# Kernel tuning notes

Hardware: AMD Instinct MI355X
Metric: run time of the kernel (lower is better)

## Reference

```python
import jax, jax.numpy as jnp
import numpy as np

B, N, K, H, G, C, P = 2, 8192, 16, 128, 256, 10, 8


def _w(key, fan_in, fan_out):
    return jax.random.normal(key, (fan_in, fan_out), jnp.float32) * (1.0 / np.sqrt(fan_in))


def setup_inputs() -> dict:
    key = jax.random.key(0)
    ks = jax.random.split(key, 24)
    inp = {
        "points": jax.random.normal(ks[0], (B, N, 3), jnp.float32),
        "normals": jax.random.normal(ks[1], (B, N, 3), jnp.float32),
        # point_encoder: Linear(6,H) -> ReLU -> Linear(H,H) -> ReLU
        "We1": _w(ks[2], 6, H), "be1": jnp.zeros((H,), jnp.float32),
        "We2": _w(ks[3], H, H), "be2": jnp.zeros((H,), jnp.float32),
        # local_mlp: Linear(2H,H) -> ReLU -> Linear(H,H) -> ReLU
        "Wl1": _w(ks[4], 2 * H, H), "bl1": jnp.zeros((H,), jnp.float32),
        "Wl2": _w(ks[5], H, H), "bl2": jnp.zeros((H,), jnp.float32),
        # context_proj: Linear(2H,G) -> ReLU
        "Wc": _w(ks[6], 2 * H, G), "bc": jnp.zeros((G,), jnp.float32),
        # classifier: Linear(2H+G,H) -> ReLU -> Linear(H,C)
        "Wk1": _w(ks[7], 2 * H + G, H), "bk1": jnp.zeros((H,), jnp.float32),
        "Wk2": _w(ks[8], H, C), "bk2": jnp.zeros((C,), jnp.float32),
        # param_head: Linear(2H+G,H) -> ReLU -> Linear(H,P)
        "Wp1": _w(ks[9], 2 * H + G, H), "bp1": jnp.zeros((H,), jnp.float32),
        "Wp2": _w(ks[10], H, P), "bp2": jnp.zeros((P,), jnp.float32),
        "k": K,
    }
    return inp


def _knn_indices(points, k):
    # squared pairwise distances (same ordering as torch.cdist); no grad needed
    pts = jax.lax.stop_gradient(points)
    sq = jnp.sum(pts * pts, axis=-1)                      # [B,N]
    d2 = sq[:, :, None] + sq[:, None, :] - 2.0 * jnp.einsum('bnc,bmc->bnm', pts, pts)
    _, idx = jax.lax.top_k(-d2, k + 1)                    # smallest k+1 distances
    return idx[:, :, 1:]                                  # drop self -> [B,N,k]


def _forward(points, normals, We1, be1, We2, be2, Wl1, bl1, Wl2, bl2,
             Wc, bc, Wk1, bk1, Wk2, bk2, Wp1, bp1, Wp2, bp2, k):
    x = jnp.concatenate([points, normals], axis=-1)       # [B,N,6]
    pf = jax.nn.relu(jax.nn.relu(x @ We1 + be1) @ We2 + be2)   # [B,N,H]

    idx = _knn_indices(points, k)                         # [B,N,k]
    nbr = jax.vmap(lambda f, i: f[i])(pf, idx)            # [B,N,k,H]
    ctr = pf[:, :, None, :]
    edge = jnp.concatenate([jnp.broadcast_to(ctr, nbr.shape), nbr - ctr], axis=-1)  # [B,N,k,2H]
    lf = jax.nn.relu(jax.nn.relu(edge @ Wl1 + bl1) @ Wl2 + bl2)
    lf = jnp.max(lf, axis=2)                              # [B,N,H]

    ctx = jax.nn.relu(jnp.concatenate([pf, lf], axis=-1) @ Wc + bc)  # [B,N,G]
    gf = jnp.max(ctx, axis=1, keepdims=True)              # [B,1,G]
    gf = jnp.broadcast_to(gf, (pf.shape[0], pf.shape[1], gf.shape[-1]))

    fused = jnp.concatenate([pf, lf, gf], axis=-1)        # [B,N,2H+G]
    logits = jax.nn.relu(fused @ Wk1 + bk1) @ Wk2 + bk2
    param_pred = jax.nn.relu(fused @ Wp1 + bp1) @ Wp2 + bp2
    return logits, param_pred


def reference(points, normals, We1, be1, We2, be2, Wl1, bl1, Wl2, bl2,
              Wc, bc, Wk1, bk1, Wk2, bk2, Wp1, bp1, Wp2, bp2, k):
    return _forward(points, normals, We1, be1, We2, be2, Wl1, bl1, Wl2, bl2,
                    Wc, bc, Wk1, bk1, Wk2, bk2, Wp1, bp1, Wp2, bp2, k)
```

## Files before the change

### kernel.cpp

```cpp
#include <hip/hip_runtime.h>

#define B_ 2
#define N_ 8192
#define NP 16384
#define K_ 16
#define H_ 128
#define KCAP 512

typedef short bf16x8 __attribute__((ext_vector_type(8)));
typedef float f32x4 __attribute__((ext_vector_type(4)));

__device__ inline unsigned short f2b(float f) {
    unsigned u = __builtin_bit_cast(unsigned, f);
    unsigned r = (u + 0x7fff + ((u >> 16) & 1)) >> 16;
    return (unsigned short)r;
}
__device__ inline bf16x8 ldb8(const unsigned short* p) {
    return *(const bf16x8*)p;
}
__device__ inline uint4 pack8(float4 a, float4 b) {
    uint4 pk;
    pk.x = (unsigned)f2b(a.x) | ((unsigned)f2b(a.y) << 16);
    pk.y = (unsigned)f2b(a.z) | ((unsigned)f2b(a.w) << 16);
    pk.z = (unsigned)f2b(b.x) | ((unsigned)f2b(b.y) << 16);
    pk.w = (unsigned)f2b(b.z) | ((unsigned)f2b(b.w) << 16);
    return pk;
}

__global__ __launch_bounds__(256) void k_h1(
    const float* __restrict__ pts, const float* __restrict__ nrm,
    const float* __restrict__ We1, const float* __restrict__ be1,
    unsigned short* __restrict__ h1, float* __restrict__ gf,
    float4* __restrict__ pts4) {
    int tid = blockIdx.x * 256 + threadIdx.x;
    if (blockIdx.x == 0) { gf[threadIdx.x] = 0.f; gf[256 + threadIdx.x] = 0.f; }
    if (tid < NP) {
        int p = tid;
        float x = pts[p * 3], y = pts[p * 3 + 1], z = pts[p * 3 + 2];
        float sq = __fadd_rn(__fadd_rn(__fmul_rn(x, x), __fmul_rn(y, y)), __fmul_rn(z, z));
        pts4[p] = make_float4(x, y, z, sq);
    }
    for (int o = tid; o < NP * 128; o += gridDim.x * 256) {
        int p = o >> 7, h = o & 127;
        float a = be1[h];
        a += pts[p * 3]     * We1[0 * 128 + h];
        a += pts[p * 3 + 1] * We1[1 * 128 + h];
        a += pts[p * 3 + 2] * We1[2 * 128 + h];
        a += nrm[p * 3]     * We1[3 * 128 + h];
        a += nrm[p * 3 + 1] * We1[4 * 128 + h];
        a += nrm[p * 3 + 2] * We1[5 * 128 + h];
        h1[o] = f2b(fmaxf(a, 0.f));
    }
}

__global__ __launch_bounds__(256) void k_prep(
    const float* __restrict__ Wl1, const float* __restrict__ bl1,
    const float* __restrict__ Wl2, const float* __restrict__ Wc,
    const float* __restrict__ Wk1, const float* __restrict__ Wp1,
    const float* __restrict__ We2,
    unsigned short* __restrict__ WuvT, float* __restrict__ bias_cat,
    unsigned short* __restrict__ Wl2T, unsigned short* __restrict__ WcT,
    unsigned short* __restrict__ Wk1T, unsigned short* __restrict__ Wp1T,
    unsigned short* __restrict__ We2T) {
    int tid = blockIdx.x * 256 + threadIdx.x;
    int stride = gridDim.x * 256;
    for (int i = tid; i < 256 * 128; i += stride) {
        int n = i >> 7, k = i & 127;
        float val = (n < 128) ? Wl1[k * 128 + n] - Wl1[(k + 128) * 128 + n]
                              : Wl1[(k + 128) * 128 + (n - 128)];
        WuvT[i] = f2b(val);
    }
    for (int i = tid; i < 256; i += stride) bias_cat[i] = (i < 128) ? bl1[i] : 0.f;
    for (int i = tid; i < 128 * 128; i += stride) {
        int n = i >> 7, k = i & 127;
        Wl2T[i] = f2b(Wl2[k * 128 + n]);
        We2T[i] = f2b(We2[k * 128 + n]);
    }
    for (int i = tid; i < 256 * 256; i += stride) {
        int n = i >> 8, k = i & 255;
        WcT[i] = f2b(Wc[k * 256 + n]);
    }
    for (int i = tid; i < 128 * 512; i += stride) {
        int n = i >> 9, k = i & 511;
        Wk1T[i] = f2b(Wk1[k * 128 + n]);
        Wp1T[i] = f2b(Wp1[k * 128 + n]);
    }
}

__global__ __launch_bounds__(256) void k_pf2(
    const unsigned short* __restrict__ h1, const unsigned short* __restrict__ We2T,
    const float* __restrict__ be2, float* __restrict__ pf) {
    int t = threadIdx.x, l = t & 63, w = t >> 6;
    int row0 = blockIdx.x * 64 + w * 16;
    f32x4 acc[8];
    #pragma unroll
    for (int nj = 0; nj < 8; ++nj) acc[nj] = (f32x4){0.f, 0.f, 0.f, 0.f};
    #pragma unroll
    for (int ks = 0; ks < 4; ++ks) {
        bf16x8 a = ldb8(&h1[(size_t)(row0 + (l & 15)) * 128 + ks * 32 + (l >> 4) * 8]);
        #pragma unroll
        for (int nj = 0; nj < 8; ++nj) {
            bf16x8 bfr = ldb8(&We2T[(size_t)(nj * 16 + (l & 15)) * 128 + ks * 32 + (l >> 4) * 8]);
            acc[nj] = __builtin_amdgcn_mfma_f32_16x16x32_bf16(a, bfr, acc[nj], 0, 0, 0);
        }
    }
    #pragma unroll
    for (int nj = 0; nj < 8; ++nj) {
        int col = nj * 16 + (l & 15);
        float bias = be2[col];
        #pragma unroll
        for (int rg = 0; rg < 4; ++rg) {
            int row = row0 + (l >> 4) * 4 + rg;
            pf[(size_t)row * 128 + col] = fmaxf(acc[nj][rg] + bias, 0.f);
        }
    }
}

__device__ inline float knn_thresh(const int* __restrict__ hh, int l) {
    int h0 = hh[4 * l], h1 = hh[4 * l + 1], h2 = hh[4 * l + 2], h3 = hh[4 * l + 3];
    int c0 = h0, c1 = c0 + h1, c2 = c1 + h2, c3 = c2 + h3;
    int tot = c3;
    int inc = tot;
    for (int off = 1; off < 64; off <<= 1) {
        int vv = __shfl_up(inc, off);
        if (l >= off) inc += vv;
    }
    int excl = inc - tot;
    int Bc = 255;
    if      (excl + c0 >= 16) Bc = 4 * l;
    else if (excl + c1 >= 16) Bc = 4 * l + 1;
    else if (excl + c2 >= 16) Bc = 4 * l + 2;
    else if (excl + c3 >= 16) Bc = 4 * l + 3;
    for (int m = 1; m < 64; m <<= 1) Bc = min(Bc, __shfl_xor(Bc, m));
    return __uint_as_float((unsigned)(Bc + 401) << 21);
}

__global__ __launch_bounds__(256) void k_knn(
    const float4* __restrict__ pts4, int* __restrict__ knn) {
    __shared__ int hist[4][260];
    __shared__ unsigned long long buf[4][KCAP];
    int t = threadIdx.x, w = t >> 6, l = t & 63;
    int b = blockIdx.x >> 11;
    int q = (blockIdx.x & 2047) * 4 + w;
    const float4* pb = pts4 + b * N_;
    float4 qp = pb[q];
    for (int i = l; i < 256; i += 64) hist[w][i] = 0;
    int cntw = 0;

    #pragma unroll 2
    for (int i = 0; i < 16; ++i) {
        int j = l + 64 * i;
        float4 c = pb[j];
        float dot = __fadd_rn(__fadd_rn(__fmul_rn(qp.x, c.x), __fmul_rn(qp.y, c.y)), __fmul_rn(qp.z, c.z));
        float d2 = __fsub_rn(__fadd_rn(qp.w, c.w), __fmul_rn(2.f, dot));
        d2 = (j == q) ? 1e30f : d2;
        unsigned uu = __float_as_uint(d2);
        int bk = (d2 < 0.f) ? 0 : min(255, max(0, (int)(uu >> 21) - 400));
        atomicAdd(&hist[w][bk], 1);
    }
    float Tf = knn_thresh(&hist[w][0], l);

    #pragma unroll 4
    for (int i = 0; i < 128; ++i) {
        int j = l + 64 * i;
        float4 c = pb[j];
        float dot = __fadd_rn(__fadd_rn(__fmul_rn(qp.x, c.x), __fmul_rn(qp.y, c.y)), __fmul_rn(qp.z, c.z));
        float d2 = __fsub_rn(__fadd_rn(qp.w, c.w), __fmul_rn(2.f, dot));
        bool take = (d2 < Tf);
        unsigned long long mask = __ballot(take);
        if (take) {
            unsigned du = __float_as_uint(d2);
            unsigned mu = du ^ (unsigned)(((int)du >> 31) | 0x80000000);
            int pos = cntw + __popcll(mask & ((1ull << l) - 1ull));
            if (pos < KCAP) buf[w][pos] = ((unsigned long long)mu << 32) | (unsigned)j;
        }
        cntw += __popcll(mask);
    }
    int m_ = min(cntw, KCAP);

    unsigned long long key[8];
    #pragma unroll
    for (int r = 0; r < 8; ++r) {
        int e = l + 64 * r;
        key[r] = (e < m_) ? buf[w][e] : ~0ull;
    }
    unsigned long long lmin = key[0];
    #pragma unroll
    for (int r = 1; r < 8; ++r) lmin = (key[r] < lmin) ? key[r] : lmin;
    int emitted = 0;
    for (int r17 = 0; r17 < 17 && emitted < 16; ++r17) {
        unsigned long long wv = lmin;
        for (int m = 1; m < 64; m <<= 1) {
            unsigned long long o = __shfl_xor(wv, m);
            wv = (o < wv) ? o : wv;
        }
        int idx = (int)(wv & 0xffffffffu);
        if (idx != q) {
            if (l == 0) knn[((size_t)b * N_ + q) * 16 + emitted] = b * N_ + idx;
            ++emitted;
        }
        if (lmin == wv) {
            #pragma unroll
            for (int r = 0; r < 8; ++r) if (key[r] == wv) key[r] = ~0ull;
            lmin = key[0];
            #pragma unroll
            for (int r = 1; r < 8; ++r) lmin = (key[r] < lmin) ? key[r] : lmin;
        }
    }
}

__global__ __launch_bounds__(256) void k_uv(
    const float* __restrict__ pf, const unsigned short* __restrict__ WuvT,
    const float* __restrict__ bias_cat,
    float* __restrict__ u, float* __restrict__ v) {
    __shared__ __align__(16) unsigned short As[128 * 136];
    int t = threadIdx.x;
    int l = t & 63, w = t >> 6;
    int wr = w >> 1, wcn = w & 1;
    int rowbase = blockIdx.x * 128;
    int ncol0 = blockIdx.y * 128;

    #pragma unroll
    for (int i = 0; i < 8; ++i) {
        int ci = t + 256 * i;
        int r = ci >> 4, c8 = (ci & 15) * 8;
        const float4* sp = (const float4*)(pf + (size_t)(rowbase + r) * 128 + c8);
        *(uint4*)&As[r * 136 + c8] = pack8(sp[0], sp[1]);
    }
    __syncthreads();

    f32x4 acc[4][4];
    #pragma unroll
    for (int i = 0; i < 4; ++i)
        #pragma unroll
        for (int j = 0; j < 4; ++j) acc[i][j] = (f32x4){0.f, 0.f, 0.f, 0.f};

    #pragma unroll
    for (int ks = 0; ks < 4; ++ks) {
        bf16x8 bfr[4], afr[4];
        #pragma unroll
        for (int nj = 0; nj < 4; ++nj)
            bfr[nj] = ldb8(&WuvT[(size_t)(ncol0 + wcn * 64 + nj * 16 + (l & 15)) * 128 + ks * 32 + (l >> 4) * 8]);
        #pragma unroll
        for (int mi = 0; mi < 4; ++mi)
            afr[mi] = ldb8(&As[(wr * 64 + mi * 16 + (l & 15)) * 136 + ks * 32 + (l >> 4) * 8]);
        #pragma unroll
        for (int mi = 0; mi < 4; ++mi)
            #pragma unroll
            for (int nj = 0; nj < 4; ++nj)
                acc[mi][nj] = __builtin_amdgcn_mfma_f32_16x16x32_bf16(afr[mi], bfr[nj], acc[mi][nj], 0, 0, 0);
    }
    float* outp = (ncol0 == 0) ? u : v;
    #pragma unroll
    for (int mi = 0; mi < 4; ++mi)
        #pragma unroll
        for (int nj = 0; nj < 4; ++nj) {
            int col = wcn * 64 + nj * 16 + (l & 15);
            float bias = bias_cat[ncol0 + col];
            #pragma unroll
            for (int rg = 0; rg < 4; ++rg) {
                int row = wr * 64 + mi * 16 + (l >> 4) * 4 + rg;
                outp[(size_t)(rowbase + row) * 128 + col] = acc[mi][nj][rg] + bias;
            }
        }
}

__global__ __launch_bounds__(256) void k_edge(
    const float* __restrict__ u, const float* __restrict__ v,
    const int* __restrict__ knn, const unsigned short* __restrict__ Wl2T,
    const float* __restrict__ bl2, float* __restrict__ lf) {
    __shared__ __align__(16) unsigned short h1s[128 * 136];
    int t = threadIdx.x;
    int l = t & 63, w = t >> 6;
    int wr = w >> 1, wcn = w & 1;
    int rowbase = blockIdx.x * 128;
    int p0 = blockIdx.x * 8;

    #pragma unroll 2
    for (int i = 0; i < 8; ++i) {
        int ci = t + 256 * i;
        int r = ci >> 4, c8 = (ci & 15) * 8;
        int nb = knn[rowbase + r];
        int pt = p0 + (r >> 4);
        const float4* vp = (const float4*)(v + (size_t)nb * 128 + c8);
        const float4* up = (const float4*)(u + (size_t)pt * 128 + c8);
        float4 va = vp[0], vb = vp[1];
        float4 ua = up[0], ub = up[1];
        unsigned d0 = (unsigned)f2b(fmaxf(ua.x + va.x, 0.f)) | ((unsigned)f2b(fmaxf(ua.y + va.y, 0.f)) << 16);
        unsigned d1 = (unsigned)f2b(fmaxf(ua.z + va.z, 0.f)) | ((unsigned)f2b(fmaxf(ua.w + va.w, 0.f)) << 16);
        unsigned d2 = (unsigned)f2b(fmaxf(ub.x + vb.x, 0.f)) | ((unsigned)f2b(fmaxf(ub.y + vb.y, 0.f)) << 16);
        unsigned d3 = (unsigned)f2b(fmaxf(ub.z + vb.z, 0.f)) | ((unsigned)f2b(fmaxf(ub.w + vb.w, 0.f)) << 16);
        uint4 pk; pk.x = d0; pk.y = d1; pk.z = d2; pk.w = d3;
        *(uint4*)&h1s[r * 136 + c8] = pk;
    }
    __syncthreads();

    f32x4 acc[4][4];
    #pragma unroll
    for (int i = 0; i < 4; ++i)
        #pragma unroll
        for (int j = 0; j < 4; ++j) acc[i][j] = (f32x4){0.f, 0.f, 0.f, 0.f};

    #pragma unroll
    for (int ks = 0; ks < 4; ++ks) {
        bf16x8 bfr[4], afr[4];
        #pragma unroll
        for (int nj = 0; nj < 4; ++nj)
            bfr[nj] = ldb8(&Wl2T[(size_t)(wcn * 64 + nj * 16 + (l & 15)) * 128 + ks * 32 + (l >> 4) * 8]);
        #pragma unroll
        for (int mi = 0; mi < 4; ++mi)
            afr[mi] = ldb8(&h1s[(wr * 64 + mi * 16 + (l & 15)) * 136 + ks * 32 + (l >> 4) * 8]);
        #pragma unroll
        for (int mi = 0; mi < 4; ++mi)
            #pragma unroll
            for (int nj = 0; nj < 4; ++nj)
                acc[mi][nj] = __builtin_amdgcn_mfma_f32_16x16x32_bf16(afr[mi], bfr[nj], acc[mi][nj], 0, 0, 0);
    }

    #pragma unroll
    for (int mi = 0; mi < 4; ++mi)
        #pragma unroll
        for (int nj = 0; nj < 4; ++nj) {
            int col = wcn * 64 + nj * 16 + (l & 15);
            float bias = bl2[col];
            float m = fmaxf(acc[mi][nj][0] + bias, 0.f);
            m = fmaxf(m, fmaxf(acc[mi][nj][1] + bias, 0.f));
            m = fmaxf(m, fmaxf(acc[mi][nj][2] + bias, 0.f));
            m = fmaxf(m, fmaxf(acc[mi][nj][3] + bias, 0.f));
            m = fmaxf(m, __shfl_xor(m, 16));
            m = fmaxf(m, __shfl_xor(m, 32));
            if (l < 16) lf[(size_t)(p0 + wr * 4 + mi) * 128 + col] = m;
        }
}

__global__ __launch_bounds__(256) void k_ctx(
    const float* __restrict__ pf, const float* __restrict__ lf,
    const unsigned short* __restrict__ WcT, const float* __restrict__ bc,
    float* __restrict__ gf) {
    __shared__ __align__(16) unsigned short As[128 * 136];
    int t = threadIdx.x;
    int l = t & 63, w = t >> 6;
    int wr = w >> 1, wcn = w & 1;
    int rowbase = blockIdx.x * 128;
    int ncol0 = blockIdx.y * 128;
    int b = rowbase >> 13;

    f32x4 acc[4][4];
    #pragma unroll
    for (int i = 0; i < 4; ++i)
        #pragma unroll
        for (int j = 0; j < 4; ++j) acc[i][j] = (f32x4){0.f, 0.f, 0.f, 0.f};

    for (int kb = 0; kb < 2; ++kb) {
        const float* src = kb ? lf : pf;
        #pragma unroll
        for (int i = 0; i < 8; ++i) {
            int ci = t + 256 * i;
            int r = ci >> 4, c8 = (ci & 15) * 8;
            const float4* sp = (const float4*)(src + (size_t)(rowbase + r) * 128 + c8);
            *(uint4*)&As[r * 136 + c8] = pack8(sp[0], sp[1]);
        }
        __syncthreads();
        #pragma unroll
        for (int ks = 0; ks < 4; ++ks) {
            bf16x8 bfr[4], afr[4];
            #pragma unroll
            for (int nj = 0; nj < 4; ++nj)
                bfr[nj] = ldb8(&WcT[(size_t)(ncol0 + wcn * 64 + nj * 16 + (l & 15)) * 256 + kb * 128 + ks * 32 + (l >> 4) * 8]);
            #pragma unroll
            for (int mi = 0; mi < 4; ++mi)
                afr[mi] = ldb8(&As[(wr * 64 + mi * 16 + (l & 15)) * 136 + ks * 32 + (l >> 4) * 8]);
            #pragma unroll
            for (int mi = 0; mi < 4; ++mi)
                #pragma unroll
                for (int nj = 0; nj < 4; ++nj)
                    acc[mi][nj] = __builtin_amdgcn_mfma_f32_16x16x32_bf16(afr[mi], bfr[nj], acc[mi][nj], 0, 0, 0);
        }
        __syncthreads();
    }
    #pragma unroll
    for (int nj = 0; nj < 4; ++nj) {
        int col = ncol0 + wcn * 64 + nj * 16 + (l & 15);
        float m = acc[0][nj][0];
        #pragma unroll
        for (int mi = 0; mi < 4; ++mi)
            #pragma unroll
            for (int rg = 0; rg < 4; ++rg) m = fmaxf(m, acc[mi][nj][rg]);
        m = fmaxf(m + bc[col], 0.f);
        m = fmaxf(m, __shfl_xor(m, 16));
        m = fmaxf(m, __shfl_xor(m, 32));
        if (l < 16) atomicMax((unsigned int*)&gf[b * 256 + col], __float_as_uint(m));
    }
}

__global__ __launch_bounds__(256) void k_head(
    const float* __restrict__ pf, const float* __restrict__ lf, const float* __restrict__ gf,
    const unsigned short* __restrict__ Wk1T, const float* __restrict__ bk1,
    const float* __restrict__ Wk2, const float* __restrict__ bk2,
    const unsigned short* __restrict__ Wp1T, const float* __restrict__ bp1,
    const float* __restrict__ Wp2, const float* __restrict__ bp2,
    float* __restrict__ out) {
    __shared__ __align__(16) char smem[67584];
    unsigned short* As = (unsigned short*)smem;
    float* hs = (float*)smem;
    int t = threadIdx.x;
    int l = t & 63, w = t >> 6;
    int wr = w >> 1, wcn = w & 1;
    int rowbase = blockIdx.x * 128;
    int b = rowbase >> 13;
    int br = blockIdx.y;
    const unsigned short* W1T = br ? Wp1T : Wk1T;
    const float* b1 = br ? bp1 : bk1;
    const float* W2 = br ? Wp2 : Wk2;
    const float* b2p = br ? bp2 : bk2;
    int OC = br ? 8 : 10;
    float* obase = out + (br ? (size_t)NP * 10 : 0);

    f32x4 acc[4][4];
    #pragma unroll
    for (int i = 0; i < 4; ++i)
        #pragma unroll
        for (int j = 0; j < 4; ++j) acc[i][j] = (f32x4){0.f, 0.f, 0.f, 0.f};

    for (int kb = 0; kb < 4; ++kb) {
        #pragma unroll
        for (int i = 0; i < 8; ++i) {
            int ci = t + 256 * i;
            int r = ci >> 4, c8 = (ci & 15) * 8;
            const float4* sp;
            if (kb == 0)      sp = (const float4*)(pf + (size_t)(rowbase + r) * 128 + c8);
            else if (kb == 1) sp = (const float4*)(lf + (size_t)(rowbase + r) * 128 + c8);
            else              sp = (const float4*)(gf + b * 256 + (kb - 2) * 128 + c8);
            *(uint4*)&As[r * 136 + c8] = pack8(sp[0], sp[1]);
        }
        __syncthreads();
        #pragma unroll
        for (int ks = 0; ks < 4; ++ks) {
            bf16x8 bfr[4], afr[4];
            #pragma unroll
            for (int nj = 0; nj < 4; ++nj)
                bfr[nj] = ldb8(&W1T[(size_t)(wcn * 64 + nj * 16 + (l & 15)) * 512 + kb * 128 + ks * 32 + (l >> 4) * 8]);
            #pragma unroll
            for (int mi = 0; mi < 4; ++mi)
                afr[mi] = ldb8(&As[(wr * 64 + mi * 16 + (l & 15)) * 136 + ks * 32 + (l >> 4) * 8]);
            #pragma unroll
            for (int mi = 0; mi < 4; ++mi)
                #pragma unroll
                for (int nj = 0; nj < 4; ++nj)
                    acc[mi][nj] = __builtin_amdgcn_mfma_f32_16x16x32_bf16(afr[mi], bfr[nj], acc[mi][nj], 0, 0, 0);
        }
        __syncthreads();
    }
    #pragma unroll
    for (int mi = 0; mi < 4; ++mi)
        #pragma unroll
        for (int nj = 0; nj < 4; ++nj)
            #pragma unroll
            for (int rg = 0; rg < 4; ++rg) {
                int row = wr * 64 + mi * 16 + (l >> 4) * 4 + rg;
                int col = wcn * 64 + nj * 16 + (l & 15);
                hs[row * 132 + col] = fmaxf(acc[mi][nj][rg] + b1[col], 0.f);
            }
    __syncthreads();
    for (int o = t; o < 128 * OC; o += 256) {
        int r = o / OC, c = o % OC;
        float a = b2p[c];
        for (int k2 = 0; k2 < 128; ++k2) a += hs[r * 132 + k2] * W2[k2 * OC + c];
        obase[(size_t)(rowbase + r) * OC + c] = a;
    }
}

extern "C" void kernel_launch(void* const* d_in, const int* in_sizes, int n_in,
                              void* d_out, int out_size, void* d_ws, size_t ws_size,
                              hipStream_t stream) {
    const float* pts = (const float*)d_in[0];
    const float* nrm = (const float*)d_in[1];
    const float* We1 = (const float*)d_in[2];
    const float* be1 = (const float*)d_in[3];
    const float* We2 = (const float*)d_in[4];
    const float* be2 = (const float*)d_in[5];
    const float* Wl1 = (const float*)d_in[6];
    const float* bl1 = (const float*)d_in[7];
    const float* Wl2 = (const float*)d_in[8];
    const float* bl2 = (const float*)d_in[9];
    const float* Wc  = (const float*)d_in[10];
    const float* bc  = (const float*)d_in[11];
    const float* Wk1 = (const float*)d_in[12];
    const float* bk1 = (const float*)d_in[13];
    const float* Wk2 = (const float*)d_in[14];
    const float* bk2 = (const float*)d_in[15];
    const float* Wp1 = (const float*)d_in[16];
    const float* bp1 = (const float*)d_in[17];
    const float* Wp2 = (const float*)d_in[18];
    const float* bp2 = (const float*)d_in[19];
    float* out = (float*)d_out;

    char* ws = (char*)d_ws;
    size_t off = 0;
    float* pf = (float*)(ws + off);       off += (size_t)NP * 128 * 4;
    float* lf = (float*)(ws + off);       off += (size_t)NP * 128 * 4;
    float* u  = (float*)(ws + off);       off += (size_t)NP * 128 * 4;
    float* v  = (float*)(ws + off);       off += (size_t)NP * 128 * 4;
    int* knn  = (int*)(ws + off);         off += (size_t)NP * 16 * 4;
    float* gf = (float*)(ws + off);       off += 2048;
    float4* pts4 = (float4*)(ws + off);   off += (size_t)NP * 16;
    float* bias_cat = (float*)(ws + off); off += 1024;
    unsigned short* WuvT = (unsigned short*)(ws + off); off += 256 * 128 * 2;
    unsigned short* Wl2T = (unsigned short*)(ws + off); off += 128 * 128 * 2;
    unsigned short* WcT  = (unsigned short*)(ws + off); off += 256 * 256 * 2;
    unsigned short* Wk1T = (unsigned short*)(ws + off); off += 128 * 512 * 2;
    unsigned short* Wp1T = (unsigned short*)(ws + off); off += 128 * 512 * 2;
    unsigned short* We2T = (unsigned short*)(ws + off); off += 128 * 128 * 2;
    unsigned short* h1   = (unsigned short*)(ws + off); off += (size_t)NP * 128 * 2;

    hipLaunchKernelGGL(k_h1, dim3(2048), dim3(256), 0, stream,
                       pts, nrm, We1, be1, h1, gf, pts4);
    hipLaunchKernelGGL(k_prep, dim3(64), dim3(256), 0, stream,
                       Wl1, bl1, Wl2, Wc, Wk1, Wp1, We2,
                       WuvT, bias_cat, Wl2T, WcT, Wk1T, Wp1T, We2T);
    hipLaunchKernelGGL(k_knn, dim3(4096), dim3(256), 0, stream, pts4, knn);
    hipLaunchKernelGGL(k_pf2, dim3(256), dim3(256), 0, stream,
                       h1, We2T, be2, pf);
    hipLaunchKernelGGL(k_uv, dim3(128, 2), dim3(256), 0, stream,
                       pf, WuvT, bias_cat, u, v);
    hipLaunchKernelGGL(k_edge, dim3(2048), dim3(256), 0, stream,
                       u, v, knn, Wl2T, bl2, lf);
    hipLaunchKernelGGL(k_ctx, dim3(128, 2), dim3(256), 0, stream,
                       pf, lf, WcT, bc, gf);
    hipLaunchKernelGGL(k_head, dim3(128, 2), dim3(256), 0, stream,
                       pf, lf, gf, Wk1T, bk1, Wk2, bk2, Wp1T, bp1, Wp2, bp2, out);
}
```

Baseline: 349.1 us.

## Store pf and lf as bf16 and load MFMA A-fragments directly from global

The intermediate per-point features pf and lf are now written in bf16 rather than fp32, which halves their storage and traffic. The downstream GEMM kernels (uv, ctx, head) no longer stage and convert them through shared memory; they load A fragments straight from global memory, and the head kernel keeps only the global feature vector in LDS. This removes barriers and conversion work, but the A loads are now strided global reads rather than LDS reads. The values were already rounded to bf16 before the MFMAs, so numerics should match.

```diff
diff --git a/kernel.cpp b/kernel.cpp
--- a/kernel.cpp
+++ b/kernel.cpp
@@ -89,7 +89,7 @@
 
 __global__ __launch_bounds__(256) void k_pf2(
     const unsigned short* __restrict__ h1, const unsigned short* __restrict__ We2T,
-    const float* __restrict__ be2, float* __restrict__ pf) {
+    const float* __restrict__ be2, unsigned short* __restrict__ pfb) {
     int t = threadIdx.x, l = t & 63, w = t >> 6;
     int row0 = blockIdx.x * 64 + w * 16;
     f32x4 acc[8];
@@ -111,7 +111,7 @@
         #pragma unroll
         for (int rg = 0; rg < 4; ++rg) {
             int row = row0 + (l >> 4) * 4 + rg;
-            pf[(size_t)row * 128 + col] = fmaxf(acc[nj][rg] + bias, 0.f);
+            pfb[(size_t)row * 128 + col] = f2b(fmaxf(acc[nj][rg] + bias, 0.f));
         }
     }
 }
@@ -210,25 +210,15 @@
 }
 
 __global__ __launch_bounds__(256) void k_uv(
-    const float* __restrict__ pf, const unsigned short* __restrict__ WuvT,
+    const unsigned short* __restrict__ pfb, const unsigned short* __restrict__ WuvT,
     const float* __restrict__ bias_cat,
     float* __restrict__ u, float* __restrict__ v) {
-    __shared__ __align__(16) unsigned short As[128 * 136];
     int t = threadIdx.x;
     int l = t & 63, w = t >> 6;
     int wr = w >> 1, wcn = w & 1;
     int rowbase = blockIdx.x * 128;
     int ncol0 = blockIdx.y * 128;
 
-    #pragma unroll
-    for (int i = 0; i < 8; ++i) {
-        int ci = t + 256 * i;
-        int r = ci >> 4, c8 = (ci & 15) * 8;
-        const float4* sp = (const float4*)(pf + (size_t)(rowbase + r) * 128 + c8);
-        *(uint4*)&As[r * 136 + c8] = pack8(sp[0], sp[1]);
-    }
-    __syncthreads();
-
     f32x4 acc[4][4];
     #pragma unroll
     for (int i = 0; i < 4; ++i)
@@ -243,7 +233,7 @@
             bfr[nj] = ldb8(&WuvT[(size_t)(ncol0 + wcn * 64 + nj * 16 + (l & 15)) * 128 + ks * 32 + (l >> 4) * 8]);
         #pragma unroll
         for (int mi = 0; mi < 4; ++mi)
-            afr[mi] = ldb8(&As[(wr * 64 + mi * 16 + (l & 15)) * 136 + ks * 32 + (l >> 4) * 8]);
+            afr[mi] = ldb8(&pfb[(size_t)(rowbase + wr * 64 + mi * 16 + (l & 15)) * 128 + ks * 32 + (l >> 4) * 8]);
         #pragma unroll
         for (int mi = 0; mi < 4; ++mi)
             #pragma unroll
@@ -268,7 +258,7 @@
 __global__ __launch_bounds__(256) void k_edge(
     const float* __restrict__ u, const float* __restrict__ v,
     const int* __restrict__ knn, const unsigned short* __restrict__ Wl2T,
-    const float* __restrict__ bl2, float* __restrict__ lf) {
+    const float* __restrict__ bl2, unsigned short* __restrict__ lfb) {
     __shared__ __align__(16) unsigned short h1s[128 * 136];
     int t = threadIdx.x;
     int l = t & 63, w = t >> 6;
@@ -329,15 +319,14 @@
             m = fmaxf(m, fmaxf(acc[mi][nj][3] + bias, 0.f));
             m = fmaxf(m, __shfl_xor(m, 16));
             m = fmaxf(m, __shfl_xor(m, 32));
-            if (l < 16) lf[(size_t)(p0 + wr * 4 + mi) * 128 + col] = m;
+            if (l < 16) lfb[(size_t)(p0 + wr * 4 + mi) * 128 + col] = f2b(m);
         }
 }
 
 __global__ __launch_bounds__(256) void k_ctx(
-    const float* __restrict__ pf, const float* __restrict__ lf,
+    const unsigned short* __restrict__ pfb, const unsigned short* __restrict__ lfb,
     const unsigned short* __restrict__ WcT, const float* __restrict__ bc,
     float* __restrict__ gf) {
-    __shared__ __align__(16) unsigned short As[128 * 136];
     int t = threadIdx.x;
     int l = t & 63, w = t >> 6;
     int wr = w >> 1, wcn = w & 1;
@@ -351,16 +340,9 @@
         #pragma unroll
         for (int j = 0; j < 4; ++j) acc[i][j] = (f32x4){0.f, 0.f, 0.f, 0.f};
 
+    #pragma unroll
     for (int kb = 0; kb < 2; ++kb) {
-        const float* src = kb ? lf : pf;
-        #pragma unroll
-        for (int i = 0; i < 8; ++i) {
-            int ci = t + 256 * i;
-            int r = ci >> 4, c8 = (ci & 15) * 8;
-            const float4* sp = (const float4*)(src + (size_t)(rowbase + r) * 128 + c8);
-            *(uint4*)&As[r * 136 + c8] = pack8(sp[0], sp[1]);
-        }
-        __syncthreads();
+        const unsigned short* srcb = kb ? lfb : pfb;
         #pragma unroll
         for (int ks = 0; ks < 4; ++ks) {
             bf16x8 bfr[4], afr[4];
@@ -369,14 +351,13 @@
                 bfr[nj] = ldb8(&WcT[(size_t)(ncol0 + wcn * 64 + nj * 16 + (l & 15)) * 256 + kb * 128 + ks * 32 + (l >> 4) * 8]);
             #pragma unroll
             for (int mi = 0; mi < 4; ++mi)
-                afr[mi] = ldb8(&As[(wr * 64 + mi * 16 + (l & 15)) * 136 + ks * 32 + (l >> 4) * 8]);
+                afr[mi] = ldb8(&srcb[(size_t)(rowbase + wr * 64 + mi * 16 + (l & 15)) * 128 + ks * 32 + (l >> 4) * 8]);
             #pragma unroll
             for (int mi = 0; mi < 4; ++mi)
                 #pragma unroll
                 for (int nj = 0; nj < 4; ++nj)
                     acc[mi][nj] = __builtin_amdgcn_mfma_f32_16x16x32_bf16(afr[mi], bfr[nj], acc[mi][nj], 0, 0, 0);
         }
-        __syncthreads();
     }
     #pragma unroll
     for (int nj = 0; nj < 4; ++nj) {
@@ -394,15 +375,15 @@
 }
 
 __global__ __launch_bounds__(256) void k_head(
-    const float* __restrict__ pf, const float* __restrict__ lf, const float* __restrict__ gf,
+    const unsigned short* __restrict__ pfb, const unsigned short* __restrict__ lfb,
+    const float* __restrict__ gf,
     const unsigned short* __restrict__ Wk1T, const float* __restrict__ bk1,
     const float* __restrict__ Wk2, const float* __restrict__ bk2,
     const unsigned short* __restrict__ Wp1T, const float* __restrict__ bp1,
     const float* __restrict__ Wp2, const float* __restrict__ bp2,
     float* __restrict__ out) {
-    __shared__ __align__(16) char smem[67584];
-    unsigned short* As = (unsigned short*)smem;
-    float* hs = (float*)smem;
+    __shared__ float hs[128 * 132];
+    __shared__ unsigned short gfs[256];
     int t = threadIdx.x;
     int l = t & 63, w = t >> 6;
     int wr = w >> 1, wcn = w & 1;
@@ -416,24 +397,17 @@
     int OC = br ? 8 : 10;
     float* obase = out + (br ? (size_t)NP * 10 : 0);
 
+    gfs[t] = f2b(gf[b * 256 + t]);
+    __syncthreads();
+
     f32x4 acc[4][4];
     #pragma unroll
     for (int i = 0; i < 4; ++i)
         #pragma unroll
         for (int j = 0; j < 4; ++j) acc[i][j] = (f32x4){0.f, 0.f, 0.f, 0.f};
 
+    #pragma unroll
     for (int kb = 0; kb < 4; ++kb) {
-        #pragma unroll
-        for (int i = 0; i < 8; ++i) {
-            int ci = t + 256 * i;
-            int r = ci >> 4, c8 = (ci & 15) * 8;
-            const float4* sp;
-            if (kb == 0)      sp = (const float4*)(pf + (size_t)(rowbase + r) * 128 + c8);
-            else if (kb == 1) sp = (const float4*)(lf + (size_t)(rowbase + r) * 128 + c8);
-            else              sp = (const float4*)(gf + b * 256 + (kb - 2) * 128 + c8);
-            *(uint4*)&As[r * 136 + c8] = pack8(sp[0], sp[1]);
-        }
-        __syncthreads();
         #pragma unroll
         for (int ks = 0; ks < 4; ++ks) {
             bf16x8 bfr[4], afr[4];
@@ -441,15 +415,20 @@
             for (int nj = 0; nj < 4; ++nj)
                 bfr[nj] = ldb8(&W1T[(size_t)(wcn * 64 + nj * 16 + (l & 15)) * 512 + kb * 128 + ks * 32 + (l >> 4) * 8]);
             #pragma unroll
-            for (int mi = 0; mi < 4; ++mi)
-                afr[mi] = ldb8(&As[(wr * 64 + mi * 16 + (l & 15)) * 136 + ks * 32 + (l >> 4) * 8]);
+            for (int mi = 0; mi < 4; ++mi) {
+                if (kb == 0)
+                    afr[mi] = ldb8(&pfb[(size_t)(rowbase + wr * 64 + mi * 16 + (l & 15)) * 128 + ks * 32 + (l >> 4) * 8]);
+                else if (kb == 1)
+                    afr[mi] = ldb8(&lfb[(size_t)(rowbase + wr * 64 + mi * 16 + (l & 15)) * 128 + ks * 32 + (l >> 4) * 8]);
+                else
+                    afr[mi] = ldb8(&gfs[(kb - 2) * 128 + ks * 32 + (l >> 4) * 8]);
+            }
             #pragma unroll
             for (int mi = 0; mi < 4; ++mi)
                 #pragma unroll
                 for (int nj = 0; nj < 4; ++nj)
                     acc[mi][nj] = __builtin_amdgcn_mfma_f32_16x16x32_bf16(afr[mi], bfr[nj], acc[mi][nj], 0, 0, 0);
         }
-        __syncthreads();
     }
     #pragma unroll
     for (int mi = 0; mi < 4; ++mi)
@@ -497,8 +476,8 @@
 
     char* ws = (char*)d_ws;
     size_t off = 0;
-    float* pf = (float*)(ws + off);       off += (size_t)NP * 128 * 4;
-    float* lf = (float*)(ws + off);       off += (size_t)NP * 128 * 4;
+    unsigned short* pfb = (unsigned short*)(ws + off); off += (size_t)NP * 128 * 2;
+    unsigned short* lfb = (unsigned short*)(ws + off); off += (size_t)NP * 128 * 2;
     float* u  = (float*)(ws + off);       off += (size_t)NP * 128 * 4;
     float* v  = (float*)(ws + off);       off += (size_t)NP * 128 * 4;
     int* knn  = (int*)(ws + off);         off += (size_t)NP * 16 * 4;
@@ -520,13 +499,13 @@
                        WuvT, bias_cat, Wl2T, WcT, Wk1T, Wp1T, We2T);
     hipLaunchKernelGGL(k_knn, dim3(4096), dim3(256), 0, stream, pts4, knn);
     hipLaunchKernelGGL(k_pf2, dim3(256), dim3(256), 0, stream,
-                       h1, We2T, be2, pf);
+                       h1, We2T, be2, pfb);
     hipLaunchKernelGGL(k_uv, dim3(128, 2), dim3(256), 0, stream,
-                       pf, WuvT, bias_cat, u, v);
+                       pfb, WuvT, bias_cat, u, v);
     hipLaunchKernelGGL(k_edge, dim3(2048), dim3(256), 0, stream,
-                       u, v, knn, Wl2T, bl2, lf);
+                       u, v, knn, Wl2T, bl2, lfb);
     hipLaunchKernelGGL(k_ctx, dim3(128, 2), dim3(256), 0, stream,
-                       pf, lf, WcT, bc, gf);
+                       pfb, lfb, WcT, bc, gf);
     hipLaunchKernelGGL(k_head, dim3(128, 2), dim3(256), 0, stream,
-                       pf, lf, gf, Wk1T, bk1, Wk2, bk2, Wp1T, bp1, Wp2, bp2, out);
-}
+                       pfb, lfb, gf, Wk1T, bk1, Wk2, bk2, Wp1T, bp1, Wp2, bp2, out);
+}
```

Measured after the change: 340.8 us. 2.4% less time.
